# Performance work log

Hardware: AMD Instinct MI355X
Metric: run time of the kernel (lower is better)

The kernel has to match this reference:

```python
import jax, jax.numpy as jnp
import numpy as np

EPS = 1e-5


def _batchnorm(x, gamma, beta):
    # training-mode BatchNorm over the point/voxel dim (axis 0)
    mean = jnp.mean(x, axis=0)
    var = jnp.var(x, axis=0)
    return (x - mean) * jax.lax.rsqrt(var + EPS) * gamma + beta


def setup_inputs() -> dict:
    N, P, NI, NF, K, I = 100000, 200000, 32, 64, 27, 8
    key = jax.random.key(0)
    ks = jax.random.split(key, 10)
    return {
        "x_feats": jax.random.normal(ks[0], (N, NI), jnp.float32),
        "z_feats": jax.random.normal(ks[1], (P, NI), jnp.float32),
        "interp_w": jax.random.uniform(ks[2], (P, I), jnp.float32),
        "nbr_idx": jax.random.randint(ks[3], (N, K), 0, N, jnp.int32),
        "interp_idx": jax.random.randint(ks[4], (P, I), 0, N, jnp.int32),
        "p2v_idx": jax.random.randint(ks[5], (P,), 0, N, jnp.int32),
        "conv1_w": jax.random.normal(ks[6], (K, NI, NF), jnp.float32) / np.float32(np.sqrt(K * NI)),
        "conv2_w": jax.random.normal(ks[7], (K, NF, NF), jnp.float32) / np.float32(np.sqrt(K * NF)),
        "bn_gamma": jnp.ones((NF,), jnp.float32),
        "bn_beta": jnp.zeros((NF,), jnp.float32),
        "pbn_gamma": jnp.ones((NI,), jnp.float32),
        "pbn_beta": jnp.zeros((NI,), jnp.float32),
        "lin_w": jax.random.normal(ks[8], (NI, NF), jnp.float32) / np.float32(np.sqrt(NI)),
        "lin_b": jnp.zeros((NF,), jnp.float32),
    }


def reference(x_feats, z_feats, interp_w, nbr_idx, interp_idx, p2v_idx,
              conv1_w, conv2_w, bn_gamma, bn_beta, pbn_gamma, pbn_beta,
              lin_w, lin_b):
    N = x_feats.shape[0]
    # --- voxel branch: Conv3d -> BN -> SiLU -> Conv3d (submanifold sparse conv
    # = neighbor gather via kernel map + grouped GEMM over 27 offsets) ---
    h = jnp.einsum('nki,kio->no', x_feats[nbr_idx], conv1_w)   # [N, NF]
    h = jax.nn.silu(_batchnorm(h, bn_gamma, bn_beta))
    x = jnp.einsum('nki,kio->no', h[nbr_idx], conv2_w)         # [N, NF]
    # --- voxel_to_point: trilinear gather from 8 surrounding voxels ---
    z1 = jnp.sum(x[interp_idx] * interp_w[..., None], axis=1)  # [P, NF]
    # --- point branch: z1.F += Linear(SiLU(BN(z.F))) ---
    pz = jax.nn.silu(_batchnorm(z_feats, pbn_gamma, pbn_beta))
    z1 = z1 + pz @ lin_w + lin_b                               # [P, NF]
    # --- point_to_voxel: scatter-average point features into voxels ---
    sums = jax.ops.segment_sum(z1, p2v_idx, num_segments=N)    # [N, NF]
    cnt = jax.ops.segment_sum(jnp.ones((z1.shape[0], 1), z1.dtype), p2v_idx,
                              num_segments=N)
    x_new = sums / jnp.maximum(cnt, 1.0)
    return (x_new, z1)
```

## Files before the change

kernel.cpp:

```cpp
#include <hip/hip_runtime.h>
#include <cstdint>

#define EPSF 1e-5f
constexpr int KOFF = 27;

typedef __attribute__((ext_vector_type(8))) short bf16x8;
typedef __attribute__((ext_vector_type(4))) float f32x4;
typedef unsigned short ushort_t;
typedef unsigned int uint_t;

__device__ __forceinline__ ushort_t f2b(float f) {
    uint_t u = __float_as_uint(f);
    u += 0x7fffu + ((u >> 16) & 1u);
    return (ushort_t)(u >> 16);
}
__device__ __forceinline__ void u4tof(uint4 u, float* f) {
    uint_t w[4] = {u.x, u.y, u.z, u.w};
#pragma unroll
    for (int i = 0; i < 4; ++i) {
        f[2 * i]     = __uint_as_float(w[i] << 16);
        f[2 * i + 1] = __uint_as_float(w[i] & 0xffff0000u);
    }
}

__device__ __forceinline__ void gload_lds16(const void* g, float* l) {
    __builtin_amdgcn_global_load_lds(
        (const __attribute__((address_space(1))) void*)g,
        (__attribute__((address_space(3))) void*)l, 16, 0, 0);
}

__global__ __launch_bounds__(256) void cvt_k(const float* __restrict__ in,
                                             ushort_t* __restrict__ out, int n8) {
    int i = blockIdx.x * 256 + threadIdx.x;
    if (i >= n8) return;
    float4 a = ((const float4*)in)[2 * i];
    float4 b = ((const float4*)in)[2 * i + 1];
    uint4 o;
    o.x = (uint_t)f2b(a.x) | ((uint_t)f2b(a.y) << 16);
    o.y = (uint_t)f2b(a.z) | ((uint_t)f2b(a.w) << 16);
    o.z = (uint_t)f2b(b.x) | ((uint_t)f2b(b.y) << 16);
    o.w = (uint_t)f2b(b.z) | ((uint_t)f2b(b.w) << 16);
    ((uint4*)out)[i] = o;
}

__global__ __launch_bounds__(256) void wtT_k(const float* __restrict__ W,
                                             ushort_t* __restrict__ Wt, int CIN) {
    int t     = blockIdx.x * 256 + threadIdx.x;
    int total = KOFF * CIN * 64;
    if (t >= total) return;
    int o    = t & 63;
    int rest = t >> 6;
    int i    = rest % CIN;
    int k    = rest / CIN;
    Wt[((size_t)k * 64 + o) * CIN + i] = f2b(W[t]);
}

__global__ __launch_bounds__(256) void linT_k(const float* __restrict__ lw,
                                              ushort_t* __restrict__ wt) {
    int t = blockIdx.x * 256 + threadIdx.x;
    if (t >= 64 * 32) return;
    int o = t >> 5, i = t & 31;
    wt[o * 32 + i] = f2b(lw[i * 64 + o]);
}

template <int CIN>
__global__ __launch_bounds__(256) void convm_k(
    const ushort_t* __restrict__ feats, const int* __restrict__ nbr,
    const ushort_t* __restrict__ Wt, ushort_t* __restrict__ outp, int N) {
    constexpr int CHUNKS = CIN / 8;
    constexpr int T      = CIN / 32;
    constexpr int NS     = CHUNKS / 4;
    constexpr int M      = CHUNKS - 1;
    constexpr int PH     = 3;
    constexpr int NPH    = KOFF / PH;

    __shared__ float lds[2][PH][64 * CHUNKS * 4];

    const int lane = threadIdx.x & 63;
    const int wv   = threadIdx.x >> 6;
    const int lo   = lane & 15;
    const int hi   = lane >> 4;
    const int row0 = blockIdx.x * 64;

    int srcoff[NS];
    const int* nbp[NS];
    int ldsbase[NS];
#pragma unroll
    for (int i = 0; i < NS; ++i) {
        int c      = (wv * NS + i) * 64 + lane;
        int r      = c / CHUNKS;
        int ch     = c & M;
        srcoff[i]  = (ch ^ (r & M)) * 8;
        int grow   = row0 + r;
        if (grow >= N) grow = N - 1;
        nbp[i]     = nbr + (size_t)grow * KOFF;
        ldsbase[i] = (wv * NS + i) * 256;
    }

    f32x4 acc[4] = {{0.f, 0.f, 0.f, 0.f},
                    {0.f, 0.f, 0.f, 0.f},
                    {0.f, 0.f, 0.f, 0.f},
                    {0.f, 0.f, 0.f, 0.f}};

    int idxb[2][PH][NS];
    bf16x8 Bb[2][PH][T];

    auto LOADIDX = [&](int pp) {
#pragma unroll
        for (int s = 0; s < PH; ++s)
#pragma unroll
            for (int i = 0; i < NS; ++i)
                idxb[pp & 1][s][i] = nbp[i][pp * PH + s];
    };
    auto LOADB = [&](int pp) {
#pragma unroll
        for (int s = 0; s < PH; ++s) {
            const ushort_t* wb =
                Wt + ((size_t)(pp * PH + s) * 64 + wv * 16 + lo) * CIN + hi * 8;
#pragma unroll
            for (int t = 0; t < T; ++t)
                Bb[pp & 1][s][t] = *(const bf16x8*)(wb + t * 32);
        }
    };
    auto STAGE = [&](int pp) {
#pragma unroll
        for (int s = 0; s < PH; ++s)
#pragma unroll
            for (int i = 0; i < NS; ++i) {
                const ushort_t* src =
                    feats + (size_t)idxb[pp & 1][s][i] * CIN + srcoff[i];
                gload_lds16(src, &lds[pp & 1][s][ldsbase[i]]);
            }
    };

    LOADIDX(0);
    LOADIDX(1);
    LOADB(0);
    STAGE(0);
    __syncthreads();

#pragma unroll
    for (int p = 0; p < NPH; ++p) {
        if (p + 2 < NPH) LOADIDX(p + 2);
        if (p + 1 < NPH) LOADB(p + 1);
        if (p + 1 < NPH) STAGE(p + 1);
        __builtin_amdgcn_sched_barrier(0);
#pragma unroll
        for (int s = 0; s < PH; ++s) {
#pragma unroll
            for (int mt = 0; mt < 4; ++mt) {
                const int R = mt * 16 + lo;
#pragma unroll
                for (int t = 0; t < T; ++t) {
                    int d    = t * 4 + hi;
                    int slot = d ^ (R & M);
                    bf16x8 a =
                        *(const bf16x8*)&lds[p & 1][s][(R * CHUNKS + slot) * 4];
                    acc[mt] = __builtin_amdgcn_mfma_f32_16x16x32_bf16(
                        a, Bb[p & 1][s][t], acc[mt], 0, 0, 0);
                }
            }
        }
        __syncthreads();
    }

#pragma unroll
    for (int mt = 0; mt < 4; ++mt) {
#pragma unroll
        for (int r = 0; r < 4; ++r) {
            int orow = row0 + mt * 16 + hi * 4 + r;
            if (orow < N)
                outp[(size_t)orow * 64 + wv * 16 + lo] = f2b(acc[mt][r]);
        }
    }
}

__global__ __launch_bounds__(256) void statsp1_k(const float* __restrict__ v,
                                                 int n, float* __restrict__ part) {
    __shared__ float ls[2 * 256];
    const int c = threadIdx.x & 31;
    int r0      = blockIdx.x * 8 + (threadIdx.x >> 5);
    int stride  = gridDim.x * 8;
    float s = 0.f, ss = 0.f;
    for (int r = r0; r < n; r += stride) {
        float x = v[(size_t)r * 32 + c];
        s += x;
        ss += x * x;
    }
    ls[threadIdx.x]       = s;
    ls[256 + threadIdx.x] = ss;
    __syncthreads();
    for (int off = 128; off >= 32; off >>= 1) {
        if (threadIdx.x < off) {
            ls[threadIdx.x] += ls[threadIdx.x + off];
            ls[256 + threadIdx.x] += ls[256 + threadIdx.x + off];
        }
        __syncthreads();
    }
    if (threadIdx.x < 32) {
        part[(size_t)blockIdx.x * 64 + threadIdx.x]      = ls[threadIdx.x];
        part[(size_t)blockIdx.x * 64 + 32 + threadIdx.x] = ls[256 + threadIdx.x];
    }
}

__global__ __launch_bounds__(256) void statsb1_k(const ushort_t* __restrict__ v,
                                                 int n, float* __restrict__ part) {
    __shared__ float ls[2][256];
    const int c8 = threadIdx.x & 7;
    int r0 = blockIdx.x * 32 + (threadIdx.x >> 3);
    float s[8], ss[8];
#pragma unroll
    for (int j = 0; j < 8; ++j) { s[j] = 0.f; ss[j] = 0.f; }
    for (int r = r0; r < n; r += gridDim.x * 32) {
        uint4 u = *(const uint4*)(v + (size_t)r * 64 + c8 * 8);
        float f[8];
        u4tof(u, f);
#pragma unroll
        for (int j = 0; j < 8; ++j) { s[j] += f[j]; ss[j] += f[j] * f[j]; }
    }
#pragma unroll
    for (int j = 0; j < 8; ++j) {
        ls[0][threadIdx.x] = s[j];
        ls[1][threadIdx.x] = ss[j];
        __syncthreads();
        for (int off = 128; off >= 8; off >>= 1) {
            if (threadIdx.x < off) {
                ls[0][threadIdx.x] += ls[0][threadIdx.x + off];
                ls[1][threadIdx.x] += ls[1][threadIdx.x + off];
            }
            __syncthreads();
        }
        if (threadIdx.x < 8) {
            part[(size_t)blockIdx.x * 128 + threadIdx.x * 8 + j]      = ls[0][threadIdx.x];
            part[(size_t)blockIdx.x * 128 + 64 + threadIdx.x * 8 + j] = ls[1][threadIdx.x];
        }
        __syncthreads();
    }
}

__global__ __launch_bounds__(128) void statsr_k(const float* __restrict__ part,
                                                float* __restrict__ out,
                                                int G, int C2) {
    int c = threadIdx.x;
    if (c >= C2) return;
    float s = 0.f;
#pragma unroll 8
    for (int g = 0; g < G; ++g) s += part[(size_t)g * C2 + c];
    out[c] = s;
}

__global__ __launch_bounds__(256) void bnsilub_k(ushort_t* __restrict__ h,
                                                 const float* __restrict__ stats,
                                                 const float* __restrict__ gamma,
                                                 const float* __restrict__ beta,
                                                 int total8, float invN) {
    int i8 = blockIdx.x * 256 + threadIdx.x;
    if (i8 >= total8) return;
    int c0  = (i8 * 8) & 63;
    uint4 u = ((const uint4*)h)[i8];
    float f[8];
    u4tof(u, f);
#pragma unroll
    for (int j = 0; j < 8; ++j) {
        int c     = c0 + j;
        float m   = stats[c] * invN;
        float var = stats[64 + c] * invN - m * m;
        float x   = (f[j] - m) * rsqrtf(var + EPSF) * gamma[c] + beta[c];
        f[j]      = x / (1.f + expf(-x));
    }
    uint4 o;
    o.x = (uint_t)f2b(f[0]) | ((uint_t)f2b(f[1]) << 16);
    o.y = (uint_t)f2b(f[2]) | ((uint_t)f2b(f[3]) << 16);
    o.z = (uint_t)f2b(f[4]) | ((uint_t)f2b(f[5]) << 16);
    o.w = (uint_t)f2b(f[6]) | ((uint_t)f2b(f[7]) << 16);
    ((uint4*)h)[i8] = o;
}

__global__ __launch_bounds__(256) void point_k(
    const ushort_t* __restrict__ x,
    const float* __restrict__ z_feats,
    const float* __restrict__ interp_w,
    const int* __restrict__ interp_idx,
    const ushort_t* __restrict__ lin_wt,
    const float* __restrict__ lin_b,
    const float* __restrict__ pstats, const float* __restrict__ pgamma,
    const float* __restrict__ pbeta, float* __restrict__ z1_out,
    int P, float invP) {
    __shared__ ushort_t pz[64 * 40];
    __shared__ float zl[64 * 68];

    const int lane = threadIdx.x & 63;
    const int wv   = threadIdx.x >> 6;
    const int lo   = lane & 15;
    const int hi   = lane >> 4;
    const int p0   = blockIdx.x * 64;

    {
        int pp = p0 + lane;
        if (pp >= P) pp = P - 1;
        const int cb      = wv;
        const float4* zr  = (const float4*)(z_feats + (size_t)pp * 32 + cb * 8);
        float4 z0 = zr[0], z1v = zr[1];
        float f[8] = {z0.x, z0.y, z0.z, z0.w, z1v.x, z1v.y, z1v.z, z1v.w};
        uint_t pk[4];
#pragma unroll
        for (int j2 = 0; j2 < 4; ++j2) {
            ushort_t lo16, hi16;
#pragma unroll
            for (int e = 0; e < 2; ++e) {
                int j     = j2 * 2 + e;
                int c     = cb * 8 + j;
                float m   = pstats[c] * invP;
                float var = pstats[32 + c] * invP - m * m;
                float zn  = (f[j] - m) * rsqrtf(var + EPSF) * pgamma[c] + pbeta[c];
                float pzv = zn / (1.f + expf(-zn));
                ushort_t b = f2b(pzv);
                if (e == 0) lo16 = b; else hi16 = b;
            }
            pk[j2] = (uint_t)lo16 | ((uint_t)hi16 << 16);
        }
        *(uint4*)&pz[lane * 40 + cb * 8] = make_uint4(pk[0], pk[1], pk[2], pk[3]);
    }
    __syncthreads();

    {
        bf16x8 a = *(const bf16x8*)&pz[(wv * 16 + lo) * 40 + hi * 8];
        f32x4 lacc[4];
#pragma unroll
        for (int nt = 0; nt < 4; ++nt) {
            bf16x8 b = *(const bf16x8*)(lin_wt + (size_t)(nt * 16 + lo) * 32 + hi * 8);
            lacc[nt] = __builtin_amdgcn_mfma_f32_16x16x32_bf16(
                a, b, (f32x4){0.f, 0.f, 0.f, 0.f}, 0, 0, 0);
        }
#pragma unroll
        for (int nt = 0; nt < 4; ++nt)
#pragma unroll
            for (int r = 0; r < 4; ++r)
                zl[(wv * 16 + hi * 4 + r) * 68 + nt * 16 + lo] = lacc[nt][r];
    }
    __syncthreads();

    const int p = p0 + lane;
    if (p >= P) return;
    const int wbase = __builtin_amdgcn_readfirstlane(wv * 16);

    const int4* iip   = (const int4*)(interp_idx + (size_t)p * 8);
    const float4* iwp = (const float4*)(interp_w + (size_t)p * 8);
    int4 ia = iip[0], ib = iip[1];
    float4 wa = iwp[0], wb = iwp[1];
    int idxs[8]  = {ia.x, ia.y, ia.z, ia.w, ib.x, ib.y, ib.z, ib.w};
    float wts[8] = {wa.x, wa.y, wa.z, wa.w, wb.x, wb.y, wb.z, wb.w};

    float acc[16];
#pragma unroll
    for (int o4 = 0; o4 < 4; ++o4) {
        f32x4 lv = *(const f32x4*)&zl[lane * 68 + wbase + o4 * 4];
#pragma unroll
        for (int j = 0; j < 4; ++j) acc[o4 * 4 + j] = lv[j];
    }

#pragma unroll
    for (int t = 0; t < 8; ++t) {
        const ushort_t* xr = x + (size_t)idxs[t] * 64 + wbase;
        float w            = wts[t];
        uint4 u0 = *(const uint4*)xr;
        uint4 u1 = *(const uint4*)(xr + 8);
        float f[16];
        u4tof(u0, f);
        u4tof(u1, f + 8);
#pragma unroll
        for (int o = 0; o < 16; ++o) acc[o] = fmaf(w, f[o], acc[o]);
    }

    const float* lb = lin_b + wbase;
#pragma unroll
    for (int o = 0; o < 16; ++o) acc[o] += lb[o];

    float* zo = z1_out + (size_t)p * 64 + wbase;
#pragma unroll
    for (int o = 0; o < 16; o += 4) {
        float4 v = {acc[o], acc[o + 1], acc[o + 2], acc[o + 3]};
        *(float4*)(zo + o) = v;
    }
}

__global__ __launch_bounds__(256) void hist_k(const int* __restrict__ p2v,
                                              int* __restrict__ cnt, int P) {
    int p = blockIdx.x * 256 + threadIdx.x;
    if (p < P) atomicAdd(&cnt[p2v[p]], 1);
}

__global__ __launch_bounds__(256) void scan1_k(const int* __restrict__ cnt,
                                               int* __restrict__ tmp,
                                               int* __restrict__ bsum, int n) {
    __shared__ int s[256];
    int i = blockIdx.x * 256 + threadIdx.x;
    int v = (i < n) ? cnt[i] : 0;
    s[threadIdx.x] = v;
    __syncthreads();
    for (int off = 1; off < 256; off <<= 1) {
        int t = (threadIdx.x >= off) ? s[threadIdx.x - off] : 0;
        __syncthreads();
        s[threadIdx.x] += t;
        __syncthreads();
    }
    if (i < n) tmp[i] = s[threadIdx.x];
    if (threadIdx.x == 255) bsum[blockIdx.x] = s[255];
}

__global__ void scan2_k(const int* __restrict__ bsum, int* __restrict__ bpre,
                        int nb) {
    if (blockIdx.x == 0 && threadIdx.x == 0) {
        int a = 0;
        for (int b = 0; b < nb; ++b) { bpre[b] = a; a += bsum[b]; }
    }
}

__global__ __launch_bounds__(256) void scan3_k(const int* __restrict__ cnt,
                                               const int* __restrict__ tmp,
                                               const int* __restrict__ bpre,
                                               int* __restrict__ off, int n) {
    int i = blockIdx.x * 256 + threadIdx.x;
    if (i < n) off[i] = bpre[i >> 8] + tmp[i] - cnt[i];
}

__global__ __launch_bounds__(256) void fill_k(const int* __restrict__ p2v,
                                              const int* __restrict__ off,
                                              int* __restrict__ cursor,
                                              int* __restrict__ bucket, int P) {
    int p = blockIdx.x * 256 + threadIdx.x;
    if (p >= P) return;
    int v    = p2v[p];
    int slot = atomicAdd(&cursor[v], 1);
    bucket[off[v] + slot] = p;
}

__global__ __launch_bounds__(256) void avg_k(const float* __restrict__ z1,
                                             const int* __restrict__ off,
                                             const int* __restrict__ cnt,
                                             const int* __restrict__ bucket,
                                             float* __restrict__ xnew, int N) {
    int tid = blockIdx.x * 256 + threadIdx.x;
    int v   = tid >> 2;
    if (v >= N) return;
    int q  = tid & 3;
    int c  = cnt[v];
    int st = off[v];
    float acc[16];
#pragma unroll
    for (int o = 0; o < 16; ++o) acc[o] = 0.f;
    for (int j = 0; j < c; ++j) {
        int p            = bucket[st + j];
        const float4* zr = (const float4*)(z1 + (size_t)p * 64 + q * 16);
#pragma unroll
        for (int c4 = 0; c4 < 4; ++c4) {
            float4 t = zr[c4];
            acc[c4 * 4 + 0] += t.x;
            acc[c4 * 4 + 1] += t.y;
            acc[c4 * 4 + 2] += t.z;
            acc[c4 * 4 + 3] += t.w;
        }
    }
    float rc  = 1.f / fmaxf((float)c, 1.f);
    float* op = xnew + (size_t)v * 64 + q * 16;
#pragma unroll
    for (int o = 0; o < 16; o += 4) {
        float4 t = {acc[o] * rc, acc[o + 1] * rc, acc[o + 2] * rc, acc[o + 3] * rc};
        *(float4*)(op + o) = t;
    }
}

extern "C" void kernel_launch(void* const* d_in, const int* in_sizes, int n_in,
                              void* d_out, int out_size, void* d_ws, size_t ws_size,
                              hipStream_t stream) {
    const float* x_feats   = (const float*)d_in[0];
    const float* z_feats   = (const float*)d_in[1];
    const float* interp_w  = (const float*)d_in[2];
    const int* nbr_idx     = (const int*)d_in[3];
    const int* interp_idx  = (const int*)d_in[4];
    const int* p2v_idx     = (const int*)d_in[5];
    const float* conv1_w   = (const float*)d_in[6];
    const float* conv2_w   = (const float*)d_in[7];
    const float* bn_gamma  = (const float*)d_in[8];
    const float* bn_beta   = (const float*)d_in[9];
    const float* pbn_gamma = (const float*)d_in[10];
    const float* pbn_beta  = (const float*)d_in[11];
    const float* lin_w     = (const float*)d_in[12];
    const float* lin_b     = (const float*)d_in[13];

    const int N  = in_sizes[3] / KOFF;
    const int P  = in_sizes[5];
    const int NB = (N + 255) / 256;
    const int GH = 512;
    const int GP = 256;

    ushort_t* h2    = (ushort_t*)d_ws;
    ushort_t* xb    = h2 + (size_t)N * 64;
    ushort_t* xf16  = xb + (size_t)N * 64;
    ushort_t* wt1   = xf16 + (size_t)N * 32;
    ushort_t* wt2   = wt1 + KOFF * 64 * 32;
    ushort_t* lwt   = wt2 + KOFF * 64 * 64;
    int* cnt        = (int*)(lwt + 64 * 32);
    int* cursor     = cnt + N;
    float* stats    = (float*)(cursor + N);
    int* tmp        = (int*)(stats + 192);
    int* off        = tmp + N;
    int* bsum       = off + N;
    int* bpre       = bsum + 512;
    int* bucket     = bpre + 512;
    float* part_h   = (float*)(bucket + P);
    float* part_p   = part_h + (size_t)GH * 128;
    float* stats_h  = stats;
    float* stats_p  = stats + 128;

    float* xnew = (float*)d_out;
    float* z1   = xnew + (size_t)N * 64;

    hipMemsetAsync(cnt, 0, (size_t)2 * N * sizeof(int), stream);

    cvt_k<<<((size_t)N * 32 / 8 + 255) / 256, 256, 0, stream>>>(x_feats, xf16,
                                                                N * 32 / 8);
    wtT_k<<<(KOFF * 32 * 64 + 255) / 256, 256, 0, stream>>>(conv1_w, wt1, 32);
    wtT_k<<<(KOFF * 64 * 64 + 255) / 256, 256, 0, stream>>>(conv2_w, wt2, 64);
    linT_k<<<8, 256, 0, stream>>>(lin_w, lwt);

    hist_k<<<(P + 255) / 256, 256, 0, stream>>>(p2v_idx, cnt, P);
    scan1_k<<<NB, 256, 0, stream>>>(cnt, tmp, bsum, N);
    scan2_k<<<1, 1, 0, stream>>>(bsum, bpre, NB);
    scan3_k<<<NB, 256, 0, stream>>>(cnt, tmp, bpre, off, N);
    fill_k<<<(P + 255) / 256, 256, 0, stream>>>(p2v_idx, off, cursor, bucket, P);

    statsp1_k<<<GP, 256, 0, stream>>>(z_feats, P, part_p);
    statsr_k<<<1, 128, 0, stream>>>(part_p, stats_p, GP, 64);

    convm_k<32><<<(N + 63) / 64, 256, 0, stream>>>(xf16, nbr_idx, wt1, h2, N);

    statsb1_k<<<GH, 256, 0, stream>>>(h2, N, part_h);
    statsr_k<<<1, 128, 0, stream>>>(part_h, stats_h, GH, 128);
    bnsilub_k<<<((size_t)N * 64 / 8 + 255) / 256, 256, 0, stream>>>(
        h2, stats_h, bn_gamma, bn_beta, N * 64 / 8, 1.f / (float)N);

    convm_k<64><<<(N + 63) / 64, 256, 0, stream>>>(h2, nbr_idx, wt2, xb, N);

    point_k<<<(P + 63) / 64, 256, 0, stream>>>(xb, z_feats, interp_w, interp_idx,
                                               lwt, lin_b, stats_p, pbn_gamma,
                                               pbn_beta, z1, P, 1.f / (float)P);

    avg_k<<<((size_t)N * 4 + 255) / 256, 256, 0, stream>>>(z1, off, cnt, bucket,
                                                           xnew, N);

    (void)n_in; (void)out_size; (void)ws_size;
}
```

Before: 316.3 us.

## Replace LDS-staged sparse conv with register-direct gather and parallel block scan

The sparse conv kernel stops staging gathered neighbor rows through LDS with async global-to-LDS loads and block barriers. Each wave now owns 16 output rows and all 64 output channels. It loads A fragments directly from global memory into registers and keeps a rotating register pipeline of A and weight fragments across the 27 offsets. This removes the LDS traffic and __syncthreads, at the cost of more register pressure and more redundant weight loads per wave. Separately, the single-thread serial scan over block sums becomes a 512-thread parallel scan, which assumes there are at most 512 blocks.

```diff
diff --git a/kernel.cpp b/kernel.cpp
--- a/kernel.cpp
+++ b/kernel.cpp
@@ -21,12 +21,6 @@
         f[2 * i]     = __uint_as_float(w[i] << 16);
         f[2 * i + 1] = __uint_as_float(w[i] & 0xffff0000u);
     }
-}
-
-__device__ __forceinline__ void gload_lds16(const void* g, float* l) {
-    __builtin_amdgcn_global_load_lds(
-        (const __attribute__((address_space(1))) void*)g,
-        (__attribute__((address_space(3))) void*)l, 16, 0, 0);
 }
 
 __global__ __launch_bounds__(256) void cvt_k(const float* __restrict__ in,
@@ -64,113 +58,77 @@
 }
 
 template <int CIN>
-__global__ __launch_bounds__(256) void convm_k(
-    const ushort_t* __restrict__ feats, const int* __restrict__ nbr,
-    const ushort_t* __restrict__ Wt, ushort_t* __restrict__ outp, int N) {
-    constexpr int CHUNKS = CIN / 8;
-    constexpr int T      = CIN / 32;
-    constexpr int NS     = CHUNKS / 4;
-    constexpr int M      = CHUNKS - 1;
-    constexpr int PH     = 3;
-    constexpr int NPH    = KOFF / PH;
-
-    __shared__ float lds[2][PH][64 * CHUNKS * 4];
-
-    const int lane = threadIdx.x & 63;
-    const int wv   = threadIdx.x >> 6;
-    const int lo   = lane & 15;
-    const int hi   = lane >> 4;
-    const int row0 = blockIdx.x * 64;
-
-    int srcoff[NS];
-    const int* nbp[NS];
-    int ldsbase[NS];
-#pragma unroll
-    for (int i = 0; i < NS; ++i) {
-        int c      = (wv * NS + i) * 64 + lane;
-        int r      = c / CHUNKS;
-        int ch     = c & M;
-        srcoff[i]  = (ch ^ (r & M)) * 8;
-        int grow   = row0 + r;
-        if (grow >= N) grow = N - 1;
-        nbp[i]     = nbr + (size_t)grow * KOFF;
-        ldsbase[i] = (wv * NS + i) * 256;
-    }
+__global__ __launch_bounds__(256) void convr_k(
+    const ushort_t* __restrict__ feats,
+    const int* __restrict__ nbr,
+    const ushort_t* __restrict__ Wt,
+    ushort_t* __restrict__ outp,
+    int N) {
+    constexpr int T = CIN / 32;
+    const int lane  = threadIdx.x & 63;
+    const int lo    = lane & 15;
+    const int hi    = lane >> 4;
+    const int row0  = blockIdx.x * 64 + (threadIdx.x >> 6) * 16;
+    const int mrow  = row0 + lo;
+    const int mrowc = mrow < N ? mrow : N - 1;
+    const int* nb   = nbr + (size_t)mrowc * KOFF;
+
+    int idx[KOFF];
+#pragma unroll
+    for (int k = 0; k < KOFF; ++k) idx[k] = nb[k];
 
     f32x4 acc[4] = {{0.f, 0.f, 0.f, 0.f},
                     {0.f, 0.f, 0.f, 0.f},
                     {0.f, 0.f, 0.f, 0.f},
                     {0.f, 0.f, 0.f, 0.f}};
 
-    int idxb[2][PH][NS];
-    bf16x8 Bb[2][PH][T];
-
-    auto LOADIDX = [&](int pp) {
-#pragma unroll
-        for (int s = 0; s < PH; ++s)
-#pragma unroll
-            for (int i = 0; i < NS; ++i)
-                idxb[pp & 1][s][i] = nbp[i][pp * PH + s];
+    bf16x8 A[4][T];
+    bf16x8 B[3][4 * T];
+
+    auto LOADA = [&](int slot, int k) {
+        const ushort_t* s = feats + (size_t)idx[k] * CIN + hi * 8;
+#pragma unroll
+        for (int t = 0; t < T; ++t) A[slot][t] = *(const bf16x8*)(s + t * 32);
     };
-    auto LOADB = [&](int pp) {
-#pragma unroll
-        for (int s = 0; s < PH; ++s) {
-            const ushort_t* wb =
-                Wt + ((size_t)(pp * PH + s) * 64 + wv * 16 + lo) * CIN + hi * 8;
+    auto LOADB = [&](int slot, int k) {
+        const ushort_t* wb = Wt + ((size_t)k * 64 + lo) * CIN + hi * 8;
+#pragma unroll
+        for (int nt = 0; nt < 4; ++nt)
 #pragma unroll
             for (int t = 0; t < T; ++t)
-                Bb[pp & 1][s][t] = *(const bf16x8*)(wb + t * 32);
-        }
+                B[slot][nt * T + t] =
+                    *(const bf16x8*)(wb + (size_t)nt * 16 * CIN + t * 32);
     };
-    auto STAGE = [&](int pp) {
-#pragma unroll
-        for (int s = 0; s < PH; ++s)
-#pragma unroll
-            for (int i = 0; i < NS; ++i) {
-                const ushort_t* src =
-                    feats + (size_t)idxb[pp & 1][s][i] * CIN + srcoff[i];
-                gload_lds16(src, &lds[pp & 1][s][ldsbase[i]]);
-            }
+    auto COMP = [&](int k) {
+        const int as = k % 4, bs = k % 3;
+#pragma unroll
+        for (int nt = 0; nt < 4; ++nt)
+#pragma unroll
+            for (int t = 0; t < T; ++t)
+                acc[nt] = __builtin_amdgcn_mfma_f32_16x16x32_bf16(
+                    A[as][t], B[bs][nt * T + t], acc[nt], 0, 0, 0);
     };
 
-    LOADIDX(0);
-    LOADIDX(1);
-    LOADB(0);
-    STAGE(0);
-    __syncthreads();
-
-#pragma unroll
-    for (int p = 0; p < NPH; ++p) {
-        if (p + 2 < NPH) LOADIDX(p + 2);
-        if (p + 1 < NPH) LOADB(p + 1);
-        if (p + 1 < NPH) STAGE(p + 1);
-        __builtin_amdgcn_sched_barrier(0);
-#pragma unroll
-        for (int s = 0; s < PH; ++s) {
-#pragma unroll
-            for (int mt = 0; mt < 4; ++mt) {
-                const int R = mt * 16 + lo;
-#pragma unroll
-                for (int t = 0; t < T; ++t) {
-                    int d    = t * 4 + hi;
-                    int slot = d ^ (R & M);
-                    bf16x8 a =
-                        *(const bf16x8*)&lds[p & 1][s][(R * CHUNKS + slot) * 4];
-                    acc[mt] = __builtin_amdgcn_mfma_f32_16x16x32_bf16(
-                        a, Bb[p & 1][s][t], acc[mt], 0, 0, 0);
-                }
-            }
-        }
-        __syncthreads();
-    }
-
-#pragma unroll
-    for (int mt = 0; mt < 4; ++mt) {
-#pragma unroll
-        for (int r = 0; r < 4; ++r) {
-            int orow = row0 + mt * 16 + hi * 4 + r;
-            if (orow < N)
-                outp[(size_t)orow * 64 + wv * 16 + lo] = f2b(acc[mt][r]);
+    LOADB(0, 0);
+    LOADB(1, 1);
+    LOADA(0, 0);
+    LOADA(1, 1);
+    LOADA(2, 2);
+
+#pragma unroll
+    for (int k = 0; k < KOFF; ++k) {
+        if (k + 2 < KOFF) LOADB((k + 2) % 3, k + 2);
+        if (k + 3 < KOFF) LOADA((k + 3) % 4, k + 3);
+        COMP(k);
+    }
+
+#pragma unroll
+    for (int r = 0; r < 4; ++r) {
+        int orow = row0 + hi * 4 + r;
+        if (orow < N) {
+#pragma unroll
+            for (int nt = 0; nt < 4; ++nt)
+                outp[(size_t)orow * 64 + nt * 16 + lo] = f2b(acc[nt][r]);
         }
     }
 }
@@ -408,12 +366,20 @@
     if (threadIdx.x == 255) bsum[blockIdx.x] = s[255];
 }
 
-__global__ void scan2_k(const int* __restrict__ bsum, int* __restrict__ bpre,
-                        int nb) {
-    if (blockIdx.x == 0 && threadIdx.x == 0) {
-        int a = 0;
-        for (int b = 0; b < nb; ++b) { bpre[b] = a; a += bsum[b]; }
-    }
+__global__ __launch_bounds__(512) void scan2_k(const int* __restrict__ bsum,
+                                               int* __restrict__ bpre, int nb) {
+    __shared__ int s[512];
+    int i = threadIdx.x;
+    int v = (i < nb) ? bsum[i] : 0;
+    s[i]  = v;
+    __syncthreads();
+    for (int off = 1; off < 512; off <<= 1) {
+        int t = (i >= off) ? s[i - off] : 0;
+        __syncthreads();
+        s[i] += t;
+        __syncthreads();
+    }
+    if (i < nb) bpre[i] = s[i] - v;
 }
 
 __global__ __launch_bounds__(256) void scan3_k(const int* __restrict__ cnt,
@@ -526,21 +492,21 @@
 
     hist_k<<<(P + 255) / 256, 256, 0, stream>>>(p2v_idx, cnt, P);
     scan1_k<<<NB, 256, 0, stream>>>(cnt, tmp, bsum, N);
-    scan2_k<<<1, 1, 0, stream>>>(bsum, bpre, NB);
+    scan2_k<<<1, 512, 0, stream>>>(bsum, bpre, NB);
     scan3_k<<<NB, 256, 0, stream>>>(cnt, tmp, bpre, off, N);
     fill_k<<<(P + 255) / 256, 256, 0, stream>>>(p2v_idx, off, cursor, bucket, P);
 
     statsp1_k<<<GP, 256, 0, stream>>>(z_feats, P, part_p);
     statsr_k<<<1, 128, 0, stream>>>(part_p, stats_p, GP, 64);
 
-    convm_k<32><<<(N + 63) / 64, 256, 0, stream>>>(xf16, nbr_idx, wt1, h2, N);
+    convr_k<32><<<(N + 63) / 64, 256, 0, stream>>>(xf16, nbr_idx, wt1, h2, N);
 
     statsb1_k<<<GH, 256, 0, stream>>>(h2, N, part_h);
     statsr_k<<<1, 128, 0, stream>>>(part_h, stats_h, GH, 128);
     bnsilub_k<<<((size_t)N * 64 / 8 + 255) / 256, 256, 0, stream>>>(
         h2, stats_h, bn_gamma, bn_beta, N * 64 / 8, 1.f / (float)N);
 
-    convm_k<64><<<(N + 63) / 64, 256, 0, stream>>>(h2, nbr_idx, wt2, xb, N);
+    convr_k<64><<<(N + 63) / 64, 256, 0, stream>>>(h2, nbr_idx, wt2, xb, N);
 
     point_k<<<(P + 63) / 64, 256, 0, stream>>>(xb, z_feats, interp_w, interp_idx,
                                                lwt, lin_b, stats_p, pbn_gamma,
```

Result: slower. 469.2 us (+48.3%).
